# Kernel tuning notes

Hardware: AMD Instinct MI355X
Metric: run time of the kernel (lower is better)

## Reference

```python
import jax, jax.numpy as jnp
import numpy as np

B, N, D = 64, 100, 32            # batch, nodes, node feature size
FE = [96, 160, 192]              # edge-MLP layer sizes
FN = [256, 256, 32]              # node-MLP layer sizes
ALPHA = 0.2                      # leaky relu slope


def _lin_init(key, fan_in, fan_out):
    kw, kb = jax.random.split(key)
    bound = 1.0 / np.sqrt(fan_in)
    w = jax.random.uniform(kw, (fan_in, fan_out), jnp.float32, -bound, bound)
    b = jax.random.uniform(kb, (fan_out,), jnp.float32, -bound, bound)
    return w, b


def setup_inputs() -> dict:
    key = jax.random.key(0)
    ks = jax.random.split(key, 7)
    d = {"x": jax.random.normal(ks[0], (B, N, D), jnp.float32)}
    fe_sizes = [2 * D] + FE                    # edge MLP: in = concat(x_i, x_j)
    fn_sizes = [FE[-1] + D] + FN               # node MLP: in = concat(agg, x)
    for li in range(3):
        w, b = _lin_init(ks[1 + li], fe_sizes[li], fe_sizes[li + 1])
        d[f"fe_w{li}"], d[f"fe_b{li}"] = w, b
    for li in range(3):
        w, b = _lin_init(ks[4 + li], fn_sizes[li], fn_sizes[li + 1])
        d[f"fn_w{li}"], d[f"fn_b{li}"] = w, b
    return d


def reference(x, fe_w0, fe_b0, fe_w1, fe_b1, fe_w2, fe_b2,
              fn_w0, fn_b0, fn_w1, fn_b1, fn_w2, fn_b2):
    b, n, d = x.shape
    lr = lambda v: jax.nn.leaky_relu(v, ALPHA)
    # fully-connected pairwise edge features: A[b,i,j] = concat(x_i, x_j)
    xi = jnp.broadcast_to(x[:, :, None, :], (b, n, n, d))
    xj = jnp.broadcast_to(x[:, None, :, :], (b, n, n, d))
    a = jnp.concatenate([xi, xj], axis=-1)          # [b, n, n, 2d]
    # edge MLP (fe): leaky relu after every layer (final_linear=False)
    a = lr(a @ fe_w0 + fe_b0)
    a = lr(a @ fe_w1 + fe_b1)
    a = lr(a @ fe_w2 + fe_b2)                       # [b, n, n, FE[-1]]
    # sum aggregation over neighbors j
    agg = jnp.sum(a, axis=2)                        # [b, n, FE[-1]]
    # node MLP (fn): final layer linear (final_linear=True)
    h = jnp.concatenate([agg, x], axis=-1)          # [b, n, FE[-1]+d]
    h = lr(h @ fn_w0 + fn_b0)
    h = lr(h @ fn_w1 + fn_b1)
    h = h @ fn_w2 + fn_b2                           # [b, n, FN[-1]]
    return h
```

## Files before the change

kernel.cpp:

```cpp
#include <hip/hip_runtime.h>

#define B_    64
#define N_    100
#define D_    32
#define F0    96
#define F1    160
#define F2    192
#define HID   256
#define FOUT  32

typedef unsigned short u16;
typedef unsigned int   u32;
typedef u16   u16x8 __attribute__((ext_vector_type(8)));
typedef u32   u32x2 __attribute__((ext_vector_type(2)));
typedef __bf16 bf16x8 __attribute__((ext_vector_type(8)));
typedef float  fx4   __attribute__((ext_vector_type(4)));

__device__ __forceinline__ u16 f2bf(float f) {
    return __builtin_bit_cast(u16, (__bf16)f);
}
__device__ __forceinline__ float lrelu(float v) { return v > 0.f ? v : 0.2f * v; }

__device__ __forceinline__ bf16x8 fragLds(const u16* p) {
    return __builtin_bit_cast(bf16x8, *(const u16x8*)p);
}
__device__ __forceinline__ bf16x8 fragGbl(const u16* __restrict__ p) {
    return __builtin_bit_cast(bf16x8, *(const u16x8*)p);
}
#define MFMA(a, b, c) __builtin_amdgcn_mfma_f32_16x16x32_bf16((a), (b), (c), 0, 0, 0)

__device__ __forceinline__ u32x2 quadPack(u32 h ) {
    u32 h1 = (u32)__shfl_xor((int)h, 1, 64);
    u32 pk = h | (h1 << 16);
    u32 pko = (u32)__shfl_xor((int)pk, 2, 64);
    return (u32x2){pk, pko};
}

#define OFF_P     0u
#define OFF_V     2457600u
#define OFF_AGG   4915200u
#define OFF_PACK  7372800u
#define PK_W1     0
#define PK_W2     15360
#define PK_N0     46080
#define PK_N1     103424
#define PK_N2     168960
#define PK_TOTAL  177152

#define PV_BLOCKS 2400
#define PACK_BLOCKS 346

__global__ __launch_bounds__(512) void prep_kernel(
    const float* __restrict__ x,
    const float* __restrict__ few0, const float* __restrict__ feb0,
    const float* __restrict__ few1, const float* __restrict__ few2,
    const float* __restrict__ fnw0, const float* __restrict__ fnw1,
    const float* __restrict__ fnw2,
    float* __restrict__ P, float* __restrict__ V, u16* __restrict__ wpack)
{
    const int blk = blockIdx.x, tid = threadIdx.x;
    if (blk < PV_BLOCKS) {
        int o = blk * 512 + tid;
        int r = o / 192, h = o - r * 192;
        const float* xr = x + r * D_;
        if (h < F0) {
            float acc = feb0[h];
            #pragma unroll
            for (int d = 0; d < D_; ++d) acc = fmaf(xr[d], few0[d * F0 + h], acc);
            P[r * F0 + h] = acc;
        } else {
            int k = h - F0;
            float acc = 0.f;
            #pragma unroll
            for (int d = 0; d < D_; ++d) acc = fmaf(xr[d], few0[(D_ + d) * F0 + k], acc);
            V[r * F0 + k] = acc;
        }
    } else {
        int p = (blk - PV_BLOCKS) * 512 + tid;
        const float* src; int start, Ncols, NT;
        if (p < PK_W2)      { start = PK_W1; src = few1; Ncols = F1;   NT = 10; }
        else if (p < PK_N0) { start = PK_W2; src = few2; Ncols = F2;   NT = 12; }
        else if (p < PK_N1) { start = PK_N0; src = fnw0; Ncols = HID;  NT = 16; }
        else if (p < PK_N2) { start = PK_N1; src = fnw1; Ncols = HID;  NT = 16; }
        else                { start = PK_N2; src = fnw2; Ncols = FOUT; NT = 2;  }
        int local = p - start;
        int j = local & 7, lane = (local >> 3) & 63, rest = local >> 9;
        int nt = rest % NT, kt = rest / NT;
        int n = 16 * nt + (lane & 15);
        int k = 32 * kt + 8 * (lane >> 4) + j;
        wpack[p] = f2bf(src[k * Ncols + n]);
    }
}

__global__ __launch_bounds__(512, 4) void edge_kernel(
    const float* __restrict__ P, const float* __restrict__ V,
    const u16* __restrict__ W1p, const u16* __restrict__ W2p,
    const float* __restrict__ feb1, const float* __restrict__ feb2,
    u16* __restrict__ agg)
{
    const int i = blockIdx.x, b = blockIdx.y;
    const int tid = threadIdx.x, ld = tid & 63, wv = tid >> 6;
    const int wn = wv & 3, wm = wv >> 2;
    const int row = b * N_ + i;

    __shared__ __align__(16) u16  sA0p[7 * 3 * 512];
    __shared__ __align__(16) u16  sA1p[7 * 5 * 512];
    __shared__ __align__(16) float sP[F0];
    __shared__ __align__(16) float sAggP[2 * F2];

    if (tid < F0) sP[tid] = P[row * F0 + tid];
    __syncthreads();

    {
        const float* Vb = V + b * N_ * F0;
        #pragma unroll
        for (int s = 0; s < 3; ++s) {
            int idx = tid + 512 * s;
            if (idx < 1344) {
                int lane = idx & 63, rest = idx >> 6;
                int kt = rest % 3, mt = rest / 3;
                int k = 32 * kt + 8 * (lane >> 4);
                int m = 16 * mt + (lane & 15);
                u16x8 w;
                if (m < N_) {
                    const float* vp = Vb + m * F0 + k;
                    fx4 v0 = *(const fx4*)(vp);
                    fx4 v1 = *(const fx4*)(vp + 4);
                    fx4 p0 = *(const fx4*)(sP + k);
                    fx4 p1 = *(const fx4*)(sP + k + 4);
                    #pragma unroll
                    for (int jj = 0; jj < 4; ++jj) {
                        w[jj]     = f2bf(lrelu(p0[jj] + v0[jj]));
                        w[4 + jj] = f2bf(lrelu(p1[jj] + v1[jj]));
                    }
                } else {
                    w = (u16x8){0, 0, 0, 0, 0, 0, 0, 0};
                }
                *(u16x8*)(sA0p + idx * 8) = w;
            }
        }
    }
    __syncthreads();

    const int mtB = wm ? 4 : 0, mtE = wm ? 7 : 4;
    const int c = ld & 15, rlo = (ld >> 4) * 4;
    const int c0 = c & ~3;

    {
        const int nCnt = (wn < 2) ? 3 : 2;
        bf16x8 bw[3][3]; float bias[3];
        #pragma unroll
        for (int t = 0; t < 3; ++t) if (t < nCnt) {
            int nt = wn + 4 * t;
            bias[t] = feb1[16 * nt + c];
            #pragma unroll
            for (int kt = 0; kt < 3; ++kt)
                bw[t][kt] = fragGbl(W1p + (size_t)((kt * 10 + nt) * 64 + ld) * 8);
        }
        for (int mt = mtB; mt < mtE; ++mt) {
            bf16x8 a[3];
            #pragma unroll
            for (int kt = 0; kt < 3; ++kt)
                a[kt] = fragLds(sA0p + ((mt * 3 + kt) * 64 + ld) * 8);
            fx4 acc[3];
            #pragma unroll
            for (int t = 0; t < 3; ++t) acc[t] = (fx4){0.f, 0.f, 0.f, 0.f};
            #pragma unroll
            for (int kt = 0; kt < 3; ++kt)
                #pragma unroll
                for (int t = 0; t < 3; ++t)
                    if (t < nCnt) acc[t] = MFMA(a[kt], bw[t][kt], acc[t]);
            #pragma unroll
            for (int t = 0; t < 3; ++t) if (t < nCnt) {
                int f = 16 * (wn + 4 * t) + c;
                int kt2 = f >> 5, lq = (f >> 3) & 3;
                u16* basep = sA1p + ((mt * 5 + kt2) * 64 + rlo + 16 * lq) * 8 + (c0 & 7);
                #pragma unroll
                for (int r = 0; r < 4; ++r) {
                    u32 h = (u32)f2bf(lrelu(acc[t][r] + bias[t]));
                    u32x2 two = quadPack(h);
                    if ((ld & 3) == 0)
                        *(u32x2*)(basep + r * 8) = two;
                }
            }
        }
    }
    __syncthreads();

    {
        bf16x8 bw[3][5]; float bias[3];
        float aggp[3] = {0.f, 0.f, 0.f};
        #pragma unroll
        for (int t = 0; t < 3; ++t) {
            int nt = wn + 4 * t;
            bias[t] = feb2[16 * nt + c];
            #pragma unroll
            for (int kt = 0; kt < 5; ++kt)
                bw[t][kt] = fragGbl(W2p + (size_t)((kt * 12 + nt) * 64 + ld) * 8);
        }
        for (int mt = mtB; mt < mtE; ++mt) {
            bf16x8 a[5];
            #pragma unroll
            for (int kt = 0; kt < 5; ++kt)
                a[kt] = fragLds(sA1p + ((mt * 5 + kt) * 64 + ld) * 8);
            fx4 acc[3];
            #pragma unroll
            for (int t = 0; t < 3; ++t) acc[t] = (fx4){0.f, 0.f, 0.f, 0.f};
            #pragma unroll
            for (int kt = 0; kt < 5; ++kt)
                #pragma unroll
                for (int t = 0; t < 3; ++t)
                    acc[t] = MFMA(a[kt], bw[t][kt], acc[t]);
            bool ok = (mt < 6) || (rlo == 0);
            if (ok) {
                #pragma unroll
                for (int t = 0; t < 3; ++t)
                    #pragma unroll
                    for (int r = 0; r < 4; ++r)
                        aggp[t] += lrelu(acc[t][r] + bias[t]);
            }
        }
        #pragma unroll
        for (int t = 0; t < 3; ++t) {
            aggp[t] += __shfl_xor(aggp[t], 16, 64);
            aggp[t] += __shfl_xor(aggp[t], 32, 64);
        }
        if (ld < 16) {
            #pragma unroll
            for (int t = 0; t < 3; ++t)
                sAggP[wm * F2 + 16 * (wn + 4 * t) + ld] = aggp[t];
        }
    }
    __syncthreads();

    if (tid < F2) {
        float v = sAggP[tid] + sAggP[F2 + tid];
        agg[(size_t)row * F2 + tid] = f2bf(v);
    }
}

__global__ __launch_bounds__(512, 4) void node_kernel(
    const u16* __restrict__ agg, const float* __restrict__ x,
    const u16* __restrict__ n0p, const u16* __restrict__ n1p,
    const u16* __restrict__ n2p,
    const float* __restrict__ fnb0, const float* __restrict__ fnb1,
    const float* __restrict__ fnb2,
    float* __restrict__ out)
{
    const int blk = blockIdx.x;
    const int tid = threadIdx.x, ld = tid & 63, wv = tid >> 6;
    const int wn = wv & 3, mt = wv >> 2;
    const int c = ld & 15, rlo = (ld >> 4) * 4;
    const int c0 = c & ~3;

    __shared__ __align__(16) u16 sH0p[2 * 7 * 512];
    __shared__ __align__(16) u16 sH1p[2 * 8 * 512];
    __shared__ __align__(16) u16 sH2p[2 * 8 * 512];

    #pragma unroll
    for (int s = 0; s < 2; ++s) {
        int idx = tid + 512 * s;
        if (idx < 896) {
            int lane = idx & 63, rest = idx >> 6;
            int kt = rest % 7, mtt = rest / 7;
            int k = 32 * kt + 8 * (lane >> 4);
            int m = 16 * mtt + (lane & 15);
            int g = 32 * blk + m;
            u16x8 w;
            if (k < F2) {
                w = *(const u16x8*)(agg + (size_t)g * F2 + k);
            } else {
                const float* xp = x + (size_t)g * D_ + (k - F2);
                fx4 v0 = *(const fx4*)xp;
                fx4 v1 = *(const fx4*)(xp + 4);
                #pragma unroll
                for (int jj = 0; jj < 4; ++jj) {
                    w[jj] = f2bf(v0[jj]); w[4 + jj] = f2bf(v1[jj]);
                }
            }
            *(u16x8*)(sH0p + idx * 8) = w;
        }
    }
    __syncthreads();

    {
        fx4 acc[4];
        #pragma unroll
        for (int t = 0; t < 4; ++t) acc[t] = (fx4){0.f, 0.f, 0.f, 0.f};
        for (int kt = 0; kt < 7; ++kt) {
            bf16x8 a = fragLds(sH0p + ((mt * 7 + kt) * 64 + ld) * 8);
            #pragma unroll
            for (int t = 0; t < 4; ++t) {
                bf16x8 bw = fragGbl(n0p + (size_t)((kt * 16 + wn + 4 * t) * 64 + ld) * 8);
                acc[t] = MFMA(a, bw, acc[t]);
            }
        }
        #pragma unroll
        for (int t = 0; t < 4; ++t) {
            int f = 16 * (wn + 4 * t) + c;
            float bias = fnb0[f];
            int kt2 = f >> 5, lq = (f >> 3) & 3;
            u16* basep = sH1p + ((mt * 8 + kt2) * 64 + rlo + 16 * lq) * 8 + (c0 & 7);
            #pragma unroll
            for (int r = 0; r < 4; ++r) {
                u32 h = (u32)f2bf(lrelu(acc[t][r] + bias));
                u32x2 two = quadPack(h);
                if ((ld & 3) == 0)
                    *(u32x2*)(basep + r * 8) = two;
            }
        }
    }
    __syncthreads();

    {
        fx4 acc[4];
        #pragma unroll
        for (int t = 0; t < 4; ++t) acc[t] = (fx4){0.f, 0.f, 0.f, 0.f};
        for (int kt = 0; kt < 8; ++kt) {
            bf16x8 a = fragLds(sH1p + ((mt * 8 + kt) * 64 + ld) * 8);
            #pragma unroll
            for (int t = 0; t < 4; ++t) {
                bf16x8 bw = fragGbl(n1p + (size_t)((kt * 16 + wn + 4 * t) * 64 + ld) * 8);
                acc[t] = MFMA(a, bw, acc[t]);
            }
        }
        #pragma unroll
        for (int t = 0; t < 4; ++t) {
            int f = 16 * (wn + 4 * t) + c;
            float bias = fnb1[f];
            int kt2 = f >> 5, lq = (f >> 3) & 3;
            u16* basep = sH2p + ((mt * 8 + kt2) * 64 + rlo + 16 * lq) * 8 + (c0 & 7);
            #pragma unroll
            for (int r = 0; r < 4; ++r) {
                u32 h = (u32)f2bf(lrelu(acc[t][r] + bias));
                u32x2 two = quadPack(h);
                if ((ld & 3) == 0)
                    *(u32x2*)(basep + r * 8) = two;
            }
        }
    }
    __syncthreads();

    if (wv < 4) {
        int mt2 = wv >> 1, nt = wv & 1;
        fx4 acc = (fx4){0.f, 0.f, 0.f, 0.f};
        for (int kt = 0; kt < 8; ++kt) {
            bf16x8 a = fragLds(sH2p + ((mt2 * 8 + kt) * 64 + ld) * 8);
            bf16x8 bw = fragGbl(n2p + (size_t)((kt * 2 + nt) * 64 + ld) * 8);
            acc = MFMA(a, bw, acc);
        }
        int f = 16 * nt + c;
        float bias = fnb2[f];
        #pragma unroll
        for (int r = 0; r < 4; ++r) {
            int g = 32 * blk + 16 * mt2 + rlo + r;
            out[(size_t)g * FOUT + f] = acc[r] + bias;
        }
    }
}

extern "C" void kernel_launch(void* const* d_in, const int* in_sizes, int n_in,
                              void* d_out, int out_size, void* d_ws, size_t ws_size,
                              hipStream_t stream) {
    const float* x    = (const float*)d_in[0];
    const float* few0 = (const float*)d_in[1];
    const float* feb0 = (const float*)d_in[2];
    const float* few1 = (const float*)d_in[3];
    const float* feb1 = (const float*)d_in[4];
    const float* few2 = (const float*)d_in[5];
    const float* feb2 = (const float*)d_in[6];
    const float* fnw0 = (const float*)d_in[7];
    const float* fnb0 = (const float*)d_in[8];
    const float* fnw1 = (const float*)d_in[9];
    const float* fnb1 = (const float*)d_in[10];
    const float* fnw2 = (const float*)d_in[11];
    const float* fnb2 = (const float*)d_in[12];

    char* w = (char*)d_ws;
    float* P    = (float*)(w + OFF_P);
    float* V    = (float*)(w + OFF_V);
    u16*   agg  = (u16*)(w + OFF_AGG);
    u16*   pack = (u16*)(w + OFF_PACK);

    prep_kernel<<<PV_BLOCKS + PACK_BLOCKS, 512, 0, stream>>>(
        x, few0, feb0, few1, few2, fnw0, fnw1, fnw2, P, V, pack);

    edge_kernel<<<dim3(N_, B_), 512, 0, stream>>>(
        P, V, pack + PK_W1, pack + PK_W2, feb1, feb2, agg);

    node_kernel<<<200, 512, 0, stream>>>(
        agg, x, pack + PK_N0, pack + PK_N1, pack + PK_N2,
        fnb0, fnb1, fnb2, (float*)d_out);
}
```

Baseline: 252.7 us.

## Pipeline edge MLP layers per row tile with swizzled double-buffered LDS

The edge kernel now splits output columns across all 8 waves instead of splitting rows between two wave groups. Layer-1 outputs for one 16-row tile go into a small double-buffered, XOR-swizzled LDS buffer while layer-2 consumes the previous tile. This shrinks LDS use and raises the launch-bounds occupancy target to 8 blocks, aiming for more resident blocks and fewer bank conflicts. The cost is a barrier per tile, weight fragments re-read from global/L1 on every tile instead of held in registers, and lrelu rewritten as fmax.

```diff
diff --git a/kernel.cpp b/kernel.cpp
--- a/kernel.cpp
+++ b/kernel.cpp
@@ -19,7 +19,7 @@
 __device__ __forceinline__ u16 f2bf(float f) {
     return __builtin_bit_cast(u16, (__bf16)f);
 }
-__device__ __forceinline__ float lrelu(float v) { return v > 0.f ? v : 0.2f * v; }
+__device__ __forceinline__ float lrelu(float v) { return fmaxf(v, 0.2f * v); }
 
 __device__ __forceinline__ bf16x8 fragLds(const u16* p) {
     return __builtin_bit_cast(bf16x8, *(const u16x8*)p);
@@ -29,7 +29,7 @@
 }
 #define MFMA(a, b, c) __builtin_amdgcn_mfma_f32_16x16x32_bf16((a), (b), (c), 0, 0, 0)
 
-__device__ __forceinline__ u32x2 quadPack(u32 h ) {
+__device__ __forceinline__ u32x2 quadPack(u32 h) {
     u32 h1 = (u32)__shfl_xor((int)h, 1, 64);
     u32 pk = h | (h1 << 16);
     u32 pko = (u32)__shfl_xor((int)pk, 2, 64);
@@ -92,7 +92,7 @@
     }
 }
 
-__global__ __launch_bounds__(512, 4) void edge_kernel(
+__global__ __launch_bounds__(512, 8) void edge_kernel(
     const float* __restrict__ P, const float* __restrict__ V,
     const u16* __restrict__ W1p, const u16* __restrict__ W2p,
     const float* __restrict__ feb1, const float* __restrict__ feb2,
@@ -100,13 +100,13 @@
 {
     const int i = blockIdx.x, b = blockIdx.y;
     const int tid = threadIdx.x, ld = tid & 63, wv = tid >> 6;
-    const int wn = wv & 3, wm = wv >> 2;
     const int row = b * N_ + i;
-
-    __shared__ __align__(16) u16  sA0p[7 * 3 * 512];
-    __shared__ __align__(16) u16  sA1p[7 * 5 * 512];
+    const int c_ = ld & 15, rlo = (ld >> 4) * 4;
+
+    __shared__ __align__(16) u16  sA0p[21 * 512];
+    __shared__ __align__(16) u16  sA1c[2 * 5 * 512];
     __shared__ __align__(16) float sP[F0];
-    __shared__ __align__(16) float sAggP[2 * F2];
+    __shared__ __align__(16) float sAgg[F2];
 
     if (tid < F0) sP[tid] = P[row * F0 + tid];
     __syncthreads();
@@ -142,101 +142,102 @@
     }
     __syncthreads();
 
-    const int mtB = wm ? 4 : 0, mtE = wm ? 7 : 4;
-    const int c = ld & 15, rlo = (ld >> 4) * 4;
-    const int c0 = c & ~3;
-
-    {
-        const int nCnt = (wn < 2) ? 3 : 2;
-        bf16x8 bw[3][3]; float bias[3];
-        #pragma unroll
-        for (int t = 0; t < 3; ++t) if (t < nCnt) {
-            int nt = wn + 4 * t;
-            bias[t] = feb1[16 * nt + c];
-            #pragma unroll
-            for (int kt = 0; kt < 3; ++kt)
-                bw[t][kt] = fragGbl(W1p + (size_t)((kt * 10 + nt) * 64 + ld) * 8);
-        }
-        for (int mt = mtB; mt < mtE; ++mt) {
-            bf16x8 a[3];
-            #pragma unroll
-            for (int kt = 0; kt < 3; ++kt)
-                a[kt] = fragLds(sA0p + ((mt * 3 + kt) * 64 + ld) * 8);
-            fx4 acc[3];
-            #pragma unroll
-            for (int t = 0; t < 3; ++t) acc[t] = (fx4){0.f, 0.f, 0.f, 0.f};
-            #pragma unroll
-            for (int kt = 0; kt < 3; ++kt)
-                #pragma unroll
-                for (int t = 0; t < 3; ++t)
-                    if (t < nCnt) acc[t] = MFMA(a[kt], bw[t][kt], acc[t]);
-            #pragma unroll
-            for (int t = 0; t < 3; ++t) if (t < nCnt) {
-                int f = 16 * (wn + 4 * t) + c;
-                int kt2 = f >> 5, lq = (f >> 3) & 3;
-                u16* basep = sA1p + ((mt * 5 + kt2) * 64 + rlo + 16 * lq) * 8 + (c0 & 7);
-                #pragma unroll
-                for (int r = 0; r < 4; ++r) {
-                    u32 h = (u32)f2bf(lrelu(acc[t][r] + bias[t]));
-                    u32x2 two = quadPack(h);
-                    if ((ld & 3) == 0)
-                        *(u32x2*)(basep + r * 8) = two;
-                }
-            }
-        }
-    }
-    __syncthreads();
-
-    {
-        bf16x8 bw[3][5]; float bias[3];
-        float aggp[3] = {0.f, 0.f, 0.f};
-        #pragma unroll
-        for (int t = 0; t < 3; ++t) {
-            int nt = wn + 4 * t;
-            bias[t] = feb2[16 * nt + c];
-            #pragma unroll
-            for (int kt = 0; kt < 5; ++kt)
-                bw[t][kt] = fragGbl(W2p + (size_t)((kt * 12 + nt) * 64 + ld) * 8);
-        }
-        for (int mt = mtB; mt < mtE; ++mt) {
-            bf16x8 a[5];
-            #pragma unroll
-            for (int kt = 0; kt < 5; ++kt)
-                a[kt] = fragLds(sA1p + ((mt * 5 + kt) * 64 + ld) * 8);
-            fx4 acc[3];
-            #pragma unroll
-            for (int t = 0; t < 3; ++t) acc[t] = (fx4){0.f, 0.f, 0.f, 0.f};
-            #pragma unroll
-            for (int kt = 0; kt < 5; ++kt)
-                #pragma unroll
-                for (int t = 0; t < 3; ++t)
-                    acc[t] = MFMA(a[kt], bw[t][kt], acc[t]);
-            bool ok = (mt < 6) || (rlo == 0);
-            if (ok) {
-                #pragma unroll
-                for (int t = 0; t < 3; ++t)
-                    #pragma unroll
-                    for (int r = 0; r < 4; ++r)
-                        aggp[t] += lrelu(acc[t][r] + bias[t]);
-            }
-        }
-        #pragma unroll
-        for (int t = 0; t < 3; ++t) {
-            aggp[t] += __shfl_xor(aggp[t], 16, 64);
-            aggp[t] += __shfl_xor(aggp[t], 32, 64);
-        }
-        if (ld < 16) {
-            #pragma unroll
-            for (int t = 0; t < 3; ++t)
-                sAggP[wm * F2 + 16 * (wn + 4 * t) + ld] = aggp[t];
-        }
-    }
-    __syncthreads();
-
-    if (tid < F2) {
-        float v = sAggP[tid] + sAggP[F2 + tid];
-        agg[(size_t)row * F2 + tid] = f2bf(v);
-    }
+    const bool hasL1B = (wv == 4 || wv == 5);
+    const int  ntL1A = wv, ntL1B = wv + 4;
+    const bool hasL2B = (wv < 4);
+    const int  ntL2A = wv, ntL2B = wv + 8;
+
+    const float bias1A = feb1[16 * ntL1A + c_];
+    const float bias1B = hasL1B ? feb1[16 * ntL1B + c_] : 0.f;
+    const float bias2A = feb2[16 * ntL2A + c_];
+    const float bias2B = hasL2B ? feb2[16 * ntL2B + c_] : 0.f;
+
+    const int a1off = (ld * 16) ^ (((ld >> 3) & 7) << 4);
+
+    float aggA = 0.f, aggB = 0.f;
+
+    auto runL1 = [&](int mt, u16* dst) {
+        fx4 aA = (fx4){0.f, 0.f, 0.f, 0.f}, aB = (fx4){0.f, 0.f, 0.f, 0.f};
+        #pragma unroll
+        for (int kt = 0; kt < 3; ++kt) {
+            bf16x8 a0 = fragLds(sA0p + ((mt * 3 + kt) * 64 + ld) * 8);
+            bf16x8 w1a = fragGbl(W1p + (size_t)((kt * 10 + ntL1A) * 64 + ld) * 8);
+            aA = MFMA(a0, w1a, aA);
+            if (hasL1B) {
+                bf16x8 w1b = fragGbl(W1p + (size_t)((kt * 10 + ntL1B) * 64 + ld) * 8);
+                aB = MFMA(a0, w1b, aB);
+            }
+        }
+        {
+            int lq = ((16 * ntL1A + c_) >> 3) & 3;
+            int S  = (((rlo >> 3) + 2 * lq) & 7) << 4;
+            char* base = (char*)dst + (ntL1A >> 1) * 1024 + (c_ & 4) * 2;
+            #pragma unroll
+            for (int r = 0; r < 4; ++r) {
+                u32 h = (u32)f2bf(lrelu(aA[r] + bias1A));
+                u32x2 two = quadPack(h);
+                int rowl = rlo + 16 * lq + r;
+                if ((ld & 3) == 0)
+                    *(u32x2*)(base + ((rowl * 16) ^ S)) = two;
+            }
+        }
+        if (hasL1B) {
+            int lq = ((16 * ntL1B + c_) >> 3) & 3;
+            int S  = (((rlo >> 3) + 2 * lq) & 7) << 4;
+            char* base = (char*)dst + (ntL1B >> 1) * 1024 + (c_ & 4) * 2;
+            #pragma unroll
+            for (int r = 0; r < 4; ++r) {
+                u32 h = (u32)f2bf(lrelu(aB[r] + bias1B));
+                u32x2 two = quadPack(h);
+                int rowl = rlo + 16 * lq + r;
+                if ((ld & 3) == 0)
+                    *(u32x2*)(base + ((rowl * 16) ^ S)) = two;
+            }
+        }
+    };
+
+    runL1(0, sA1c);
+    __syncthreads();
+
+    for (int p = 0; p < 7; ++p) {
+        if (p < 6) runL1(p + 1, sA1c + ((p + 1) & 1) * 2560);
+
+        fx4 cA = (fx4){0.f, 0.f, 0.f, 0.f}, cB = (fx4){0.f, 0.f, 0.f, 0.f};
+        const char* rb = (const char*)sA1c + (p & 1) * 5120 + a1off;
+        #pragma unroll
+        for (int kt = 0; kt < 5; ++kt) {
+            bf16x8 a1 = fragLds((const u16*)(rb + kt * 1024));
+            bf16x8 w2a = fragGbl(W2p + (size_t)((kt * 12 + ntL2A) * 64 + ld) * 8);
+            cA = MFMA(a1, w2a, cA);
+            if (hasL2B) {
+                bf16x8 w2b = fragGbl(W2p + (size_t)((kt * 12 + ntL2B) * 64 + ld) * 8);
+                cB = MFMA(a1, w2b, cB);
+            }
+        }
+        if ((p < 6) || (rlo == 0)) {
+            #pragma unroll
+            for (int r = 0; r < 4; ++r) {
+                aggA += lrelu(cA[r] + bias2A);
+                if (hasL2B) aggB += lrelu(cB[r] + bias2B);
+            }
+        }
+        __syncthreads();
+    }
+
+    aggA += __shfl_xor(aggA, 16, 64);
+    aggA += __shfl_xor(aggA, 32, 64);
+    if (hasL2B) {
+        aggB += __shfl_xor(aggB, 16, 64);
+        aggB += __shfl_xor(aggB, 32, 64);
+    }
+    if (ld < 16) {
+        sAgg[16 * ntL2A + ld] = aggA;
+        if (hasL2B) sAgg[16 * ntL2B + ld] = aggB;
+    }
+    __syncthreads();
+
+    if (tid < F2)
+        agg[(size_t)row * F2 + tid] = f2bf(sAgg[tid]);
 }
 
 __global__ __launch_bounds__(512, 4) void node_kernel(
@@ -379,16 +380,16 @@
     char* w = (char*)d_ws;
     float* P    = (float*)(w + OFF_P);
     float* V    = (float*)(w + OFF_V);
-    u16*   agg  = (u16*)(w + OFF_AGG);
+    u16*   aggb = (u16*)(w + OFF_AGG);
     u16*   pack = (u16*)(w + OFF_PACK);
 
     prep_kernel<<<PV_BLOCKS + PACK_BLOCKS, 512, 0, stream>>>(
         x, few0, feb0, few1, few2, fnw0, fnw1, fnw2, P, V, pack);
 
     edge_kernel<<<dim3(N_, B_), 512, 0, stream>>>(
-        P, V, pack + PK_W1, pack + PK_W2, feb1, feb2, agg);
+        P, V, pack + PK_W1, pack + PK_W2, feb1, feb2, aggb);
 
     node_kernel<<<200, 512, 0, stream>>>(
-        agg, x, pack + PK_N0, pack + PK_N1, pack + PK_N2,
+        aggb, x, pack + PK_N0, pack + PK_N1, pack + PK_N2,
         fnb0, fnb1, fnb2, (float*)d_out);
 }
```

Result: slower. 381.8 us (+51.1%).

## Split edge layers into two phases with smaller swizzled LDS buffer

Applied to the files above, without the earlier changes.

The edge kernel now runs layer 1 and layer 2 in two phases of up to 4 row tiles each. This shrinks the intermediate LDS buffer from 7 to 4 tiles, and the launch bound is raised from 4 to 6 blocks per CU so more blocks can be resident. The layer-1 output is stored with an XOR swizzle to reduce LDS bank conflicts, and leaky relu becomes an fmax. The price is an extra pair of barriers per block and reloading the weight fragments for each phase, and the tighter launch bound may force register spills.

```diff
diff --git a/kernel.cpp b/kernel.cpp
--- a/kernel.cpp
+++ b/kernel.cpp
@@ -19,7 +19,7 @@
 __device__ __forceinline__ u16 f2bf(float f) {
     return __builtin_bit_cast(u16, (__bf16)f);
 }
-__device__ __forceinline__ float lrelu(float v) { return v > 0.f ? v : 0.2f * v; }
+__device__ __forceinline__ float lrelu(float v) { return fmaxf(v, 0.2f * v); }
 
 __device__ __forceinline__ bf16x8 fragLds(const u16* p) {
     return __builtin_bit_cast(bf16x8, *(const u16x8*)p);
@@ -29,7 +29,7 @@
 }
 #define MFMA(a, b, c) __builtin_amdgcn_mfma_f32_16x16x32_bf16((a), (b), (c), 0, 0, 0)
 
-__device__ __forceinline__ u32x2 quadPack(u32 h ) {
+__device__ __forceinline__ u32x2 quadPack(u32 h) {
     u32 h1 = (u32)__shfl_xor((int)h, 1, 64);
     u32 pk = h | (h1 << 16);
     u32 pko = (u32)__shfl_xor((int)pk, 2, 64);
@@ -92,7 +92,7 @@
     }
 }
 
-__global__ __launch_bounds__(512, 4) void edge_kernel(
+__global__ __launch_bounds__(512, 6) void edge_kernel(
     const float* __restrict__ P, const float* __restrict__ V,
     const u16* __restrict__ W1p, const u16* __restrict__ W2p,
     const float* __restrict__ feb1, const float* __restrict__ feb2,
@@ -102,9 +102,10 @@
     const int tid = threadIdx.x, ld = tid & 63, wv = tid >> 6;
     const int wn = wv & 3, wm = wv >> 2;
     const int row = b * N_ + i;
-
-    __shared__ __align__(16) u16  sA0p[7 * 3 * 512];
-    __shared__ __align__(16) u16  sA1p[7 * 5 * 512];
+    const int c_ = ld & 15, rlo = (ld >> 4) * 4;
+
+    __shared__ __align__(16) u16  sA0p[21 * 512];
+    __shared__ __align__(16) u16  sA1h[4 * 5 * 512];
     __shared__ __align__(16) float sP[F0];
     __shared__ __align__(16) float sAggP[2 * F2];
 
@@ -142,94 +143,102 @@
     }
     __syncthreads();
 
-    const int mtB = wm ? 4 : 0, mtE = wm ? 7 : 4;
-    const int c = ld & 15, rlo = (ld >> 4) * 4;
-    const int c0 = c & ~3;
-
-    {
-        const int nCnt = (wn < 2) ? 3 : 2;
-        bf16x8 bw[3][3]; float bias[3];
-        #pragma unroll
-        for (int t = 0; t < 3; ++t) if (t < nCnt) {
-            int nt = wn + 4 * t;
-            bias[t] = feb1[16 * nt + c];
-            #pragma unroll
-            for (int kt = 0; kt < 3; ++kt)
-                bw[t][kt] = fragGbl(W1p + (size_t)((kt * 10 + nt) * 64 + ld) * 8);
-        }
-        for (int mt = mtB; mt < mtE; ++mt) {
-            bf16x8 a[3];
-            #pragma unroll
-            for (int kt = 0; kt < 3; ++kt)
-                a[kt] = fragLds(sA0p + ((mt * 3 + kt) * 64 + ld) * 8);
-            fx4 acc[3];
-            #pragma unroll
-            for (int t = 0; t < 3; ++t) acc[t] = (fx4){0.f, 0.f, 0.f, 0.f};
-            #pragma unroll
-            for (int kt = 0; kt < 3; ++kt)
-                #pragma unroll
-                for (int t = 0; t < 3; ++t)
-                    if (t < nCnt) acc[t] = MFMA(a[kt], bw[t][kt], acc[t]);
-            #pragma unroll
-            for (int t = 0; t < 3; ++t) if (t < nCnt) {
-                int f = 16 * (wn + 4 * t) + c;
-                int kt2 = f >> 5, lq = (f >> 3) & 3;
-                u16* basep = sA1p + ((mt * 5 + kt2) * 64 + rlo + 16 * lq) * 8 + (c0 & 7);
-                #pragma unroll
-                for (int r = 0; r < 4; ++r) {
-                    u32 h = (u32)f2bf(lrelu(acc[t][r] + bias[t]));
-                    u32x2 two = quadPack(h);
-                    if ((ld & 3) == 0)
-                        *(u32x2*)(basep + r * 8) = two;
+    const int nCnt1 = (wn < 2) ? 3 : 2;
+    const int a1off = (ld * 16) ^ (((ld >> 3) & 7) << 4);
+    float aggp[3] = {0.f, 0.f, 0.f};
+
+    for (int ph = 0; ph < 2; ++ph) {
+        const int mtb = (ph ? 4 : 0) + 2 * wm;
+        const int mte = ph ? (wm ? 7 : 6) : (mtb + 2);
+
+        {
+            bf16x8 bw[3][3]; float bias[3];
+            #pragma unroll
+            for (int t = 0; t < 3; ++t) if (t < nCnt1) {
+                int nt = wn + 4 * t;
+                bias[t] = feb1[16 * nt + c_];
+                #pragma unroll
+                for (int kt = 0; kt < 3; ++kt)
+                    bw[t][kt] = fragGbl(W1p + (size_t)((kt * 10 + nt) * 64 + ld) * 8);
+            }
+            for (int mt = mtb; mt < mte; ++mt) {
+                bf16x8 a[3];
+                #pragma unroll
+                for (int kt = 0; kt < 3; ++kt)
+                    a[kt] = fragLds(sA0p + ((mt * 3 + kt) * 64 + ld) * 8);
+                fx4 acc[3];
+                #pragma unroll
+                for (int t = 0; t < 3; ++t) acc[t] = (fx4){0.f, 0.f, 0.f, 0.f};
+                #pragma unroll
+                for (int kt = 0; kt < 3; ++kt)
+                    #pragma unroll
+                    for (int t = 0; t < 3; ++t)
+                        if (t < nCnt1) acc[t] = MFMA(a[kt], bw[t][kt], acc[t]);
+                #pragma unroll
+                for (int t = 0; t < 3; ++t) if (t < nCnt1) {
+                    int nt = wn + 4 * t;
+                    int f = 16 * nt + c_;
+                    int lq = (f >> 3) & 3;
+                    int S  = (((rlo >> 3) + 2 * lq) & 7) << 4;
+                    char* base = (char*)sA1h + (mt & 3) * 5120 + (nt >> 1) * 1024 + (c_ & 4) * 2;
+                    #pragma unroll
+                    for (int r = 0; r < 4; ++r) {
+                        u32 h = (u32)f2bf(lrelu(acc[t][r] + bias[t]));
+                        u32x2 two = quadPack(h);
+                        int rowl = rlo + 16 * lq + r;
+                        if ((ld & 3) == 0)
+                            *(u32x2*)(base + ((rowl * 16) ^ S)) = two;
+                    }
                 }
             }
         }
-    }
-    __syncthreads();
-
-    {
-        bf16x8 bw[3][5]; float bias[3];
-        float aggp[3] = {0.f, 0.f, 0.f};
-        #pragma unroll
-        for (int t = 0; t < 3; ++t) {
-            int nt = wn + 4 * t;
-            bias[t] = feb2[16 * nt + c];
-            #pragma unroll
-            for (int kt = 0; kt < 5; ++kt)
-                bw[t][kt] = fragGbl(W2p + (size_t)((kt * 12 + nt) * 64 + ld) * 8);
-        }
-        for (int mt = mtB; mt < mtE; ++mt) {
-            bf16x8 a[5];
-            #pragma unroll
-            for (int kt = 0; kt < 5; ++kt)
-                a[kt] = fragLds(sA1p + ((mt * 5 + kt) * 64 + ld) * 8);
-            fx4 acc[3];
-            #pragma unroll
-            for (int t = 0; t < 3; ++t) acc[t] = (fx4){0.f, 0.f, 0.f, 0.f};
-            #pragma unroll
-            for (int kt = 0; kt < 5; ++kt)
-                #pragma unroll
-                for (int t = 0; t < 3; ++t)
-                    acc[t] = MFMA(a[kt], bw[t][kt], acc[t]);
-            bool ok = (mt < 6) || (rlo == 0);
-            if (ok) {
-                #pragma unroll
-                for (int t = 0; t < 3; ++t)
+        __syncthreads();
+
+        {
+            bf16x8 bw[3][5]; float bias[3];
+            #pragma unroll
+            for (int t = 0; t < 3; ++t) {
+                int nt = wn + 4 * t;
+                bias[t] = feb2[16 * nt + c_];
+                #pragma unroll
+                for (int kt = 0; kt < 5; ++kt)
+                    bw[t][kt] = fragGbl(W2p + (size_t)((kt * 12 + nt) * 64 + ld) * 8);
+            }
+            for (int mt = mtb; mt < mte; ++mt) {
+                bf16x8 a[5];
+                const char* rb = (const char*)sA1h + (mt & 3) * 5120 + a1off;
+                #pragma unroll
+                for (int kt = 0; kt < 5; ++kt)
+                    a[kt] = fragLds((const u16*)(rb + kt * 1024));
+                fx4 acc[3];
+                #pragma unroll
+                for (int t = 0; t < 3; ++t) acc[t] = (fx4){0.f, 0.f, 0.f, 0.f};
+                #pragma unroll
+                for (int kt = 0; kt < 5; ++kt)
                     #pragma unroll
-                    for (int r = 0; r < 4; ++r)
-                        aggp[t] += lrelu(acc[t][r] + bias[t]);
-            }
-        }
-        #pragma unroll
-        for (int t = 0; t < 3; ++t) {
-            aggp[t] += __shfl_xor(aggp[t], 16, 64);
-            aggp[t] += __shfl_xor(aggp[t], 32, 64);
-        }
-        if (ld < 16) {
-            #pragma unroll
-            for (int t = 0; t < 3; ++t)
-                sAggP[wm * F2 + 16 * (wn + 4 * t) + ld] = aggp[t];
-        }
+                    for (int t = 0; t < 3; ++t)
+                        acc[t] = MFMA(a[kt], bw[t][kt], acc[t]);
+                if ((mt < 6) || (rlo == 0)) {
+                    #pragma unroll
+                    for (int t = 0; t < 3; ++t)
+                        #pragma unroll
+                        for (int r = 0; r < 4; ++r)
+                            aggp[t] += lrelu(acc[t][r] + bias[t]);
+                }
+            }
+        }
+        __syncthreads();
+    }
+
+    #pragma unroll
+    for (int t = 0; t < 3; ++t) {
+        aggp[t] += __shfl_xor(aggp[t], 16, 64);
+        aggp[t] += __shfl_xor(aggp[t], 32, 64);
+    }
+    if (ld < 16) {
+        #pragma unroll
+        for (int t = 0; t < 3; ++t)
+            sAggP[wm * F2 + 16 * (wn + 4 * t) + ld] = aggp[t];
     }
     __syncthreads();
 
@@ -379,16 +388,16 @@
     char* w = (char*)d_ws;
     float* P    = (float*)(w + OFF_P);
     float* V    = (float*)(w + OFF_V);
-    u16*   agg  = (u16*)(w + OFF_AGG);
+    u16*   aggb = (u16*)(w + OFF_AGG);
     u16*   pack = (u16*)(w + OFF_PACK);
 
     prep_kernel<<<PV_BLOCKS + PACK_BLOCKS, 512, 0, stream>>>(
         x, few0, feb0, few1, few2, fnw0, fnw1, fnw2, P, V, pack);
 
     edge_kernel<<<dim3(N_, B_), 512, 0, stream>>>(
-        P, V, pack + PK_W1, pack + PK_W2, feb1, feb2, agg);
+        P, V, pack + PK_W1, pack + PK_W2, feb1, feb2, aggb);
 
     node_kernel<<<200, 512, 0, stream>>>(
-        agg, x, pack + PK_N0, pack + PK_N1, pack + PK_N2,
+        aggb, x, pack + PK_N0, pack + PK_N1, pack + PK_N2,
         fnb0, fnb1, fnb2, (float*)d_out);
 }
```

New measurement: 641.3 us. 2.54x slower.
